# Performance work log

Hardware: AMD Instinct MI355X
Metric: run time of the kernel (lower is better)

## Reference

```python
import jax, jax.numpy as jnp
import numpy as np

# Static dims (match init_kwargs / input_specs)
N, F, C, H, W = 1, 60, 31, 64, 64
DIM = 60          # embed dim == F
WS = 8            # window_size
NH = 6            # num_heads
HD = DIM // NH    # head dim = 10
SHIFT = WS // 2   # shift for odd blocks
NWIN_TOK = WS * WS
MLP_HID = 4 * DIM
EPS = 1e-5


def _rel_pos_index(ws):
    # standard Swin relative position index, computed once in numpy
    coords = np.stack(np.meshgrid(np.arange(ws), np.arange(ws), indexing='ij'))  # (2, ws, ws)
    coords = coords.reshape(2, -1)                                                # (2, ws*ws)
    rel = coords[:, :, None] - coords[:, None, :]                                 # (2, n, n)
    rel = rel.transpose(1, 2, 0)
    rel[..., 0] += ws - 1
    rel[..., 1] += ws - 1
    rel[..., 0] *= 2 * ws - 1
    return rel.sum(-1)                                                            # (n, n)

RPI = jnp.asarray(_rel_pos_index(WS))  # (64, 64) int


def _attn_mask(h, w, ws, shift):
    # mask for shifted-window attention: -100 where tokens come from different regions
    img = np.zeros((h, w))
    cnt = 0
    for hs in (slice(0, -ws), slice(-ws, -shift), slice(-shift, None)):
        for wsl in (slice(0, -ws), slice(-ws, -shift), slice(-shift, None)):
            img[hs, wsl] = cnt
            cnt += 1
    m = img.reshape(h // ws, ws, w // ws, ws).transpose(0, 2, 1, 3).reshape(-1, ws * ws)  # (nW, n)
    diff = m[:, None, :] - m[:, :, None]
    return jnp.asarray(np.where(diff != 0, -100.0, 0.0).astype(np.float32))               # (nW, n, n)

ATTN_MASK = _attn_mask(H, W, WS, SHIFT)


def _ln(x, g, b):
    mu = jnp.mean(x, axis=-1, keepdims=True)
    var = jnp.mean(jnp.square(x - mu), axis=-1, keepdims=True)
    return (x - mu) * jax.lax.rsqrt(var + EPS) * g + b


def _swin_block(x, shift, g1, b1, qkv_w, qkv_b, rpb, proj_w, proj_b,
                g2, b2, fc1_w, fc1_b, fc2_w, fc2_b):
    # x: (B, L=H*W, DIM)
    B = x.shape[0]
    shortcut = x
    h = _ln(x, g1, b1).reshape(B, H, W, DIM)
    if shift > 0:
        h = jnp.roll(h, (-shift, -shift), axis=(1, 2))
    # window partition -> (B*nW, n, DIM)
    win = h.reshape(B, H // WS, WS, W // WS, WS, DIM).transpose(0, 1, 3, 2, 4, 5)
    win = win.reshape(-1, NWIN_TOK, DIM)
    Bw = win.shape[0]
    # qkv projection (torch Linear: y = x @ W.T + b)
    qkv = win @ qkv_w.T + qkv_b                                   # (Bw, n, 3*DIM)
    qkv = qkv.reshape(Bw, NWIN_TOK, 3, NH, HD).transpose(2, 0, 3, 1, 4)
    q, k, v = qkv[0], qkv[1], qkv[2]                              # (Bw, NH, n, HD)
    scale = HD ** -0.5
    attn = jnp.einsum('bhnd,bhmd->bhnm', q * scale, k)            # (Bw, NH, n, n)
    bias = rpb[RPI.reshape(-1)].reshape(NWIN_TOK, NWIN_TOK, NH).transpose(2, 0, 1)
    attn = attn + bias[None]
    if shift > 0:
        nW = ATTN_MASK.shape[0]
        attn = attn.reshape(-1, nW, NH, NWIN_TOK, NWIN_TOK) + ATTN_MASK[None, :, None]
        attn = attn.reshape(-1, NH, NWIN_TOK, NWIN_TOK)
    attn = jax.nn.softmax(attn, axis=-1)
    out = jnp.einsum('bhnm,bhmd->bhnd', attn, v).transpose(0, 2, 1, 3).reshape(Bw, NWIN_TOK, DIM)
    out = out @ proj_w.T + proj_b
    # window reverse -> (B, H, W, DIM)
    out = out.reshape(B, H // WS, W // WS, WS, WS, DIM).transpose(0, 1, 3, 2, 4, 5)
    out = out.reshape(B, H, W, DIM)
    if shift > 0:
        out = jnp.roll(out, (shift, shift), axis=(1, 2))
    x = shortcut + out.reshape(B, H * W, DIM)
    # MLP with exact GELU (torch nn.GELU default)
    h2 = _ln(x, g2, b2)
    h2 = jax.nn.gelu(h2 @ fc1_w.T + fc1_b, approximate=False) @ fc2_w.T + fc2_b
    return x + h2


def setup_inputs() -> dict:
    key = jax.random.key(0)
    ks = jax.random.split(key, 16)
    s = 0.02
    inp = {
        'x': jax.random.normal(ks[0], (N, F, C, H, W), jnp.float32),
        'norm1_g': jnp.ones((2, DIM), jnp.float32),
        'norm1_b': jnp.zeros((2, DIM), jnp.float32),
        'qkv_w': jax.random.normal(ks[1], (2, 3 * DIM, DIM), jnp.float32) * s,
        'qkv_b': jnp.zeros((2, 3 * DIM), jnp.float32),
        'rpb': jax.random.normal(ks[2], (2, (2 * WS - 1) ** 2, NH), jnp.float32) * s,
        'proj_w': jax.random.normal(ks[3], (2, DIM, DIM), jnp.float32) * s,
        'proj_b': jnp.zeros((2, DIM), jnp.float32),
        'norm2_g': jnp.ones((2, DIM), jnp.float32),
        'norm2_b': jnp.zeros((2, DIM), jnp.float32),
        'fc1_w': jax.random.normal(ks[4], (2, MLP_HID, DIM), jnp.float32) * s,
        'fc1_b': jnp.zeros((2, MLP_HID), jnp.float32),
        'fc2_w': jax.random.normal(ks[5], (2, DIM, MLP_HID), jnp.float32) * s,
        'fc2_b': jnp.zeros((2, DIM), jnp.float32),
    }
    return inp


def reference(x, norm1_g, norm1_b, qkv_w, qkv_b, rpb, proj_w, proj_b,
              norm2_g, norm2_b, fc1_w, fc1_b, fc2_w, fc2_b):
    # (N, F, C, H, W) -> (N*C, F, H, W) -> patch embed (flatten) -> (B, L, DIM)
    out = jnp.transpose(x, (0, 2, 1, 3, 4)).reshape(N * C, F, H, W)
    out = out.reshape(N * C, F, H * W).transpose(0, 2, 1)  # (B, L, DIM)
    for i in range(2):
        shift = 0 if i % 2 == 0 else SHIFT
        out = _swin_block(out, shift,
                          norm1_g[i], norm1_b[i], qkv_w[i], qkv_b[i], rpb[i],
                          proj_w[i], proj_b[i], norm2_g[i], norm2_b[i],
                          fc1_w[i], fc1_b[i], fc2_w[i], fc2_b[i])
    # patch unembed -> (B, F, H, W) -> (N, C, F, H, W) -> transpose(1,2)
    out = out.transpose(0, 2, 1).reshape(N * C, F, H, W)
    out = out.reshape(N, C, F, H, W)
    return jnp.transpose(out, (0, 2, 1, 3, 4))
```

## Files before the change

kernel.cpp:

```cpp
#include <hip/hip_runtime.h>
#include <math.h>


#define NB 31
#define NTOK 4096
#define DIM 60
#define NTOT (NB*NTOK)
#define QK_SCALE 0.31622776601683794f

typedef __attribute__((ext_vector_type(8))) short bf16x8;
typedef __attribute__((ext_vector_type(4))) float f32x4;

__device__ __forceinline__ short f2b(float f){
    union{float f;unsigned u;}v; v.f=f;
    unsigned r=(v.u+0x7FFFu+((v.u>>16)&1u))>>16; return (short)r;
}
__device__ __forceinline__ float b2f(unsigned short u){
    union{unsigned u;float f;}v; v.u=((unsigned)u)<<16; return v.f;
}
__device__ __forceinline__ unsigned pk2(float a,float b){
    return (unsigned)(unsigned short)f2b(a) | ((unsigned)(unsigned short)f2b(b)<<16);
}

#define MFMA16(a,b,c) __builtin_amdgcn_mfma_f32_16x16x32_bf16(a,b,c,0,0,0)

#define PK_QKV   0
#define PK_PROJ  13824
#define PK_W1    18432
#define PK_W2    35712
#define PK_BIAS  52608
#define PK_STRIDE 150912

__global__ __launch_bounds__(256) void pack_w(
    const float* __restrict__ qkv_w, const float* __restrict__ proj_w,
    const float* __restrict__ fc1_w, const float* __restrict__ fc2_w,
    const float* __restrict__ rpb, short* __restrict__ pk)
{
    const int L = blockIdx.x;
    short* o = pk + (size_t)L * PK_STRIDE;
    const float* qw = qkv_w + L * 10800;
    const float* pw = proj_w + L * 3600;
    const float* w1 = fc1_w + L * 14400;
    const float* w2 = fc2_w + L * 14400;
    const float* rp = rpb + L * 1350;
    const int t0 = blockIdx.y * 256 + threadIdx.x;
    const int STP = 256 * 8;

    for (int i = t0; i < 192 * 72; i += STP) {
        int row = i / 72, k = i - row * 72;
        int p = row / 96, rg = row - p * 96;
        short v = 0;
        if (rg < 90 && k < 60) {
            int which = rg / 30, idx = rg - which * 30;
            int h = p * 3 + idx / 10, e = idx - (idx / 10) * 10;
            v = f2b(qw[(which * 60 + h * 10 + e) * 60 + k]);
        }
        o[PK_QKV + i] = v;
    }
    for (int i = t0; i < 64 * 72; i += STP) {
        int n = i / 72, k = i - n * 72;
        o[PK_PROJ + i] = (n < 60 && k < 60) ? f2b(pw[n * 60 + k]) : (short)0;
    }
    for (int i = t0; i < 240 * 72; i += STP) {
        int n = i / 72, k = i - n * 72;
        o[PK_W1 + i] = (k < 60) ? f2b(w1[n * 60 + k]) : (short)0;
    }
    for (int i = t0; i < 64 * 264; i += STP) {
        int n = i / 264, k = i - n * 264;
        o[PK_W2 + i] = (n < 60 && k < 240) ? f2b(w2[n * 240 + k]) : (short)0;
    }
    for (int i = t0; i < 4 * 6 * 4096; i += STP) {
        int c = i >> 14, rem = i & 16383;
        int h = rem >> 12; rem &= 4095;
        int j = rem >> 6, ii = rem & 63;
        int iy = ii >> 3, ix = ii & 7, jy = j >> 3, jx = j & 7;
        float v = rp[((iy - jy + 7) * 15 + (ix - jx + 7)) * 6 + h];
        int wyv = (c & 2) ? 7 : 0, wxv = (c & 1) ? 7 : 0;
        int riy = wyv < 7 ? 0 : (iy < 4 ? 1 : 2);
        int rix = wxv < 7 ? 0 : (ix < 4 ? 1 : 2);
        int rjy = wyv < 7 ? 0 : (jy < 4 ? 1 : 2);
        int rjx = wxv < 7 ? 0 : (jx < 4 ? 1 : 2);
        if (riy * 3 + rix != rjy * 3 + rjx) v -= 100.f;
        o[PK_BIAS + i] = f2b(v);
    }
}

template<int L>
__global__ __launch_bounds__(256, 4) void swin_layer(
    const void* __restrict__ xin_v, void* __restrict__ xout_v,
    const float* __restrict__ g1, const float* __restrict__ b1,
    const float* __restrict__ g2, const float* __restrict__ b2,
    const short* __restrict__ pk,
    const float* __restrict__ qkv_b, const float* __restrict__ proj_b,
    const float* __restrict__ fc1_b, const float* __restrict__ fc2_b)
{
    __shared__ __attribute__((aligned(16))) short S[19328];
    short (*xnY)[72]  = (short(*)[72]) S;
    short (*qk2)[104] = (short(*)[104])(S + 4608);
    short (*vTf)[72]  = (short(*)[72]) (S + 11264);
    short (*oac)[72]  = (short(*)[72]) (S + 14720);
    short (*hb)[136]  = (short(*)[136])(S + 4608);
    short (*ln2)[72]  = oac;

    const bf16x8 Z8 = {0,0,0,0,0,0,0,0};
    const f32x4  Z4 = {0.f,0.f,0.f,0.f};

    const int tid = threadIdx.x, blk = blockIdx.x;
    const int b = blk >> 6, w = blk & 63, wy = w >> 3, wx = w & 7;
    const int shift = L ? 4 : 0;
    const int cls = L ? (((wy == 7) ? 2 : 0) + ((wx == 7) ? 1 : 0)) : 0;

    const float* xf = (const float*)xin_v;
    const unsigned short* xb = (const unsigned short*)xin_v;

    for (int i = tid; i < 64 * 36; i += 256) {
        int row = i / 36, z = i - row * 36;
        int bc = z / 6, rem = z - bc * 6;
        qk2[row][bc * 16 + 10 + rem] = 0;
    }
    for (int i = tid; i < 128; i += 256) {
        int row = i >> 1;
        *(int*)&oac[row][60 + ((i & 1) << 1)] = 0;
    }
    {
        const int tk = tid >> 2, l4 = tid & 3;
        const int ty = tk >> 3, tx = tk & 7;
        const int tok = (((wy * 8 + ty + shift) & 63) << 6) + ((wx * 8 + tx + shift) & 63);
        float xr[15]; float s = 0.f, s2 = 0.f;
#pragma unroll
        for (int dd = 0; dd < 15; ++dd) {
            float v;
            if (L == 0) v = xf[(size_t)(dd * 4 + l4) * NTOT + b * NTOK + tok];
            else        v = b2f(xb[((size_t)b * NTOK + tok) * DIM + dd * 4 + l4]);
            xr[dd] = v; s += v; s2 += v * v;
        }
        s  += __shfl_xor(s, 1);  s  += __shfl_xor(s, 2);
        s2 += __shfl_xor(s2, 1); s2 += __shfl_xor(s2, 2);
        const float mu = s * (1.f / 60.f);
        const float rs = rsqrtf(s2 * (1.f / 60.f) - mu * mu + 1e-5f);
#pragma unroll
        for (int dd = 0; dd < 15; ++dd) {
            int d = dd * 4 + l4;
            xnY[tk][d] = f2b((xr[dd] - mu) * rs * g1[d] + b1[d]);
        }
#pragma unroll
        for (int u = 0; u < 3; ++u) xnY[tk][60 + l4 * 3 + u] = 0;
    }

    const int lane = tid & 63;
    const int r16 = lane & 15, g = lane >> 4;
    const int m0 = (tid >> 6) << 4;

    int tok4[4];
#pragma unroll
    for (int r = 0; r < 4; ++r) {
        int row = m0 + g * 4 + r;
        tok4[r] = (((wy * 8 + (row >> 3) + shift) & 63) << 6)
                + ((wx * 8 + (row & 7) + shift) & 63);
    }

    bf16x8 a0 = *(const bf16x8*)&xnY[m0 + r16][g * 8];
    bf16x8 a1 = *(const bf16x8*)&xnY[m0 + r16][32 + g * 8];

    const unsigned short* bbase =
        (const unsigned short*)(pk + PK_BIAS) + cls * 24576 + (m0 + r16) + g * 256;

    for (int p = 0; p < 2; ++p) {
#pragma unroll
        for (int nt = 0; nt < 6; ++nt) {
            const short* wr = pk + PK_QKV + (size_t)(p * 96 + nt * 16 + r16) * 72;
            bf16x8 w0 = *(const bf16x8*)(wr + g * 8);
            bf16x8 w1v = *(const bf16x8*)(wr + 32 + g * 8);
            f32x4 acc = MFMA16(a0, w0, Z4);
            acc = MFMA16(a1, w1v, acc);
            int c = nt * 16 + r16;
            if (c < 90) {
                int which = c / 30, idx = c - which * 30;
                int hl = idx / 10, e = idx - hl * 10;
                float bias = qkv_b[which * 60 + (p * 3 + hl) * 10 + e];
                if (which == 0) {
#pragma unroll
                    for (int r = 0; r < 4; ++r)
                        qk2[m0 + g * 4 + r][hl * 16 + e] = f2b((acc[r] + bias) * QK_SCALE);
                } else if (which == 1) {
#pragma unroll
                    for (int r = 0; r < 4; ++r)
                        qk2[m0 + g * 4 + r][48 + hl * 16 + e] = f2b(acc[r] + bias);
                } else {
#pragma unroll
                    for (int r = 0; r < 2; ++r)
                        *(unsigned*)&vTf[hl * 16 + e][m0 + g * 4 + r * 2] =
                            pk2(acc[r * 2] + bias, acc[r * 2 + 1] + bias);
                }
            }
        }
        __syncthreads();

        for (int hl = 0; hl < 3; ++hl) {
            const int h = p * 3 + hl;
            bf16x8 qa = Z8;
            if (g < 2) qa = *(const bf16x8*)&qk2[m0 + r16][hl * 16 + g * 8];
            f32x4 sv[4];
#pragma unroll
            for (int nt = 0; nt < 4; ++nt) {
                bf16x8 kb = Z8;
                if (g < 2) kb = *(const bf16x8*)&qk2[nt * 16 + r16][48 + hl * 16 + g * 8];
                sv[nt] = MFMA16(kb, qa, Z4);
            }
            const unsigned short* bp = bbase + h * 4096;
#pragma unroll
            for (int nt = 0; nt < 4; ++nt)
#pragma unroll
                for (int r = 0; r < 4; ++r)
                    sv[nt][r] += b2f(bp[nt * 1024 + r * 64]);
            float mx = -1e30f;
#pragma unroll
            for (int nt = 0; nt < 4; ++nt)
#pragma unroll
                for (int r = 0; r < 4; ++r) mx = fmaxf(mx, sv[nt][r]);
            mx = fmaxf(mx, __shfl_xor(mx, 16));
            mx = fmaxf(mx, __shfl_xor(mx, 32));
            float sum = 0.f;
#pragma unroll
            for (int nt = 0; nt < 4; ++nt)
#pragma unroll
                for (int r = 0; r < 4; ++r) {
                    float e = __expf(sv[nt][r] - mx);
                    sv[nt][r] = e; sum += e;
                }
            sum += __shfl_xor(sum, 16);
            sum += __shfl_xor(sum, 32);
            const float inv = 1.f / sum;
            unsigned qd00 = pk2(sv[0][0], sv[0][1]), qd01 = pk2(sv[0][2], sv[0][3]);
            unsigned qd10 = pk2(sv[1][0], sv[1][1]), qd11 = pk2(sv[1][2], sv[1][3]);
            unsigned qd20 = pk2(sv[2][0], sv[2][1]), qd21 = pk2(sv[2][2], sv[2][3]);
            unsigned qd30 = pk2(sv[3][0], sv[3][1]), qd31 = pk2(sv[3][2], sv[3][3]);
            const int sA = (r16 + ((g & 1) << 5)) << 2;
            const int sB = sA + 64;
            const bool hi = (g >> 1) & 1;
            union { unsigned u[4]; bf16x8 v; } pb0, pb1;
            {
                unsigned x0 = __builtin_amdgcn_ds_bpermute(sA, (int)qd00);
                unsigned y0 = __builtin_amdgcn_ds_bpermute(sA, (int)qd10);
                pb0.u[0] = hi ? y0 : x0;
                unsigned x1 = __builtin_amdgcn_ds_bpermute(sA, (int)qd01);
                unsigned y1 = __builtin_amdgcn_ds_bpermute(sA, (int)qd11);
                pb0.u[1] = hi ? y1 : x1;
                unsigned x2 = __builtin_amdgcn_ds_bpermute(sB, (int)qd00);
                unsigned y2 = __builtin_amdgcn_ds_bpermute(sB, (int)qd10);
                pb0.u[2] = hi ? y2 : x2;
                unsigned x3 = __builtin_amdgcn_ds_bpermute(sB, (int)qd01);
                unsigned y3 = __builtin_amdgcn_ds_bpermute(sB, (int)qd11);
                pb0.u[3] = hi ? y3 : x3;
                unsigned u0 = __builtin_amdgcn_ds_bpermute(sA, (int)qd20);
                unsigned v0 = __builtin_amdgcn_ds_bpermute(sA, (int)qd30);
                pb1.u[0] = hi ? v0 : u0;
                unsigned u1 = __builtin_amdgcn_ds_bpermute(sA, (int)qd21);
                unsigned v1 = __builtin_amdgcn_ds_bpermute(sA, (int)qd31);
                pb1.u[1] = hi ? v1 : u1;
                unsigned u2 = __builtin_amdgcn_ds_bpermute(sB, (int)qd20);
                unsigned v2 = __builtin_amdgcn_ds_bpermute(sB, (int)qd30);
                pb1.u[2] = hi ? v2 : u2;
                unsigned u3 = __builtin_amdgcn_ds_bpermute(sB, (int)qd21);
                unsigned v3 = __builtin_amdgcn_ds_bpermute(sB, (int)qd31);
                pb1.u[3] = hi ? v3 : u3;
            }
            bf16x8 va0 = *(const bf16x8*)&vTf[hl * 16 + r16][g * 8];
            bf16x8 va1 = *(const bf16x8*)&vTf[hl * 16 + r16][32 + g * 8];
            f32x4 o = MFMA16(va0, pb0.v, Z4);
            o = MFMA16(va1, pb1.v, o);
            if (g < 2) {
                *(unsigned*)&oac[m0 + r16][h * 10 + g * 4]     = pk2(o[0] * inv, o[1] * inv);
                *(unsigned*)&oac[m0 + r16][h * 10 + g * 4 + 2] = pk2(o[2] * inv, o[3] * inv);
            } else if (g == 2) {
                *(unsigned*)&oac[m0 + r16][h * 10 + 8] = pk2(o[0] * inv, o[1] * inv);
            }
        }
        __syncthreads();
    }

    {
        bf16x8 oa0 = *(const bf16x8*)&oac[m0 + r16][g * 8];
        bf16x8 oa1 = *(const bf16x8*)&oac[m0 + r16][32 + g * 8];
#pragma unroll
        for (int nt = 0; nt < 4; ++nt) {
            const short* wr = pk + PK_PROJ + (size_t)(nt * 16 + r16) * 72;
            bf16x8 w0 = *(const bf16x8*)(wr + g * 8);
            bf16x8 w1v = *(const bf16x8*)(wr + 32 + g * 8);
            f32x4 acc = MFMA16(oa0, w0, Z4);
            acc = MFMA16(oa1, w1v, acc);
            int d = nt * 16 + r16;
            if (d < 60) {
                float bias = proj_b[d];
#pragma unroll
                for (int r = 0; r < 4; ++r) {
                    float res;
                    if (L == 0) res = xf[(size_t)d * NTOT + b * NTOK + tok4[r]];
                    else        res = b2f(xb[((size_t)b * NTOK + tok4[r]) * DIM + d]);
                    xnY[m0 + g * 4 + r][d] = f2b(res + acc[r] + bias);
                }
            }
        }
    }

    {
        const int tk = tid >> 2, l4 = tid & 3;
        float yr[15]; float s = 0.f, s2 = 0.f;
#pragma unroll
        for (int dd = 0; dd < 15; ++dd) {
            float v = b2f((unsigned short)xnY[tk][dd * 4 + l4]);
            yr[dd] = v; s += v; s2 += v * v;
        }
        s  += __shfl_xor(s, 1);  s  += __shfl_xor(s, 2);
        s2 += __shfl_xor(s2, 1); s2 += __shfl_xor(s2, 2);
        const float mu = s * (1.f / 60.f);
        const float rs = rsqrtf(s2 * (1.f / 60.f) - mu * mu + 1e-5f);
#pragma unroll
        for (int dd = 0; dd < 15; ++dd) {
            int d = dd * 4 + l4;
            ln2[tk][d] = f2b((yr[dd] - mu) * rs * g2[d] + b2[d]);
        }
#pragma unroll
        for (int u = 0; u < 3; ++u) ln2[tk][60 + l4 * 3 + u] = 0;
    }
    __syncthreads();

    bf16x8 la0 = *(const bf16x8*)&ln2[m0 + r16][g * 8];
    bf16x8 la1 = *(const bf16x8*)&ln2[m0 + r16][32 + g * 8];
    f32x4 acc2[4];
#pragma unroll
    for (int nt = 0; nt < 4; ++nt) acc2[nt] = Z4;

#pragma unroll
    for (int nt = 0; nt < 8; ++nt) {
        const short* wr = pk + PK_W1 + (size_t)(nt * 16 + r16) * 72;
        bf16x8 w0 = *(const bf16x8*)(wr + g * 8);
        bf16x8 w1v = *(const bf16x8*)(wr + 32 + g * 8);
        f32x4 acc = MFMA16(la0, w0, Z4);
        acc = MFMA16(la1, w1v, acc);
        int c = nt * 16 + r16;
        float bias = fc1_b[c];
#pragma unroll
        for (int r = 0; r < 4; ++r) {
            float u = acc[r] + bias;
            float zz = 1.5957691216057308f * u + 0.07135481178528657f * (u * u * u);
            float ge = u * __builtin_amdgcn_rcpf(1.f + __expf(-zz));
            hb[m0 + g * 4 + r][c] = f2b(ge);
        }
    }
#pragma unroll
    for (int kk = 0; kk < 4; ++kk) {
        bf16x8 ha = *(const bf16x8*)&hb[m0 + r16][kk * 32 + g * 8];
#pragma unroll
        for (int nt = 0; nt < 4; ++nt) {
            const short* wr = pk + PK_W2 + (size_t)(nt * 16 + r16) * 264 + kk * 32 + g * 8;
            acc2[nt] = MFMA16(ha, *(const bf16x8*)wr, acc2[nt]);
        }
    }
    *(int*)&hb[m0 + r16][112 + g * 4]     = 0;
    *(int*)&hb[m0 + r16][112 + g * 4 + 2] = 0;
#pragma unroll
    for (int nt = 0; nt < 7; ++nt) {
        const short* wr = pk + PK_W1 + (size_t)(128 + nt * 16 + r16) * 72;
        bf16x8 w0 = *(const bf16x8*)(wr + g * 8);
        bf16x8 w1v = *(const bf16x8*)(wr + 32 + g * 8);
        f32x4 acc = MFMA16(la0, w0, Z4);
        acc = MFMA16(la1, w1v, acc);
        int c = nt * 16 + r16;
        float bias = fc1_b[128 + c];
#pragma unroll
        for (int r = 0; r < 4; ++r) {
            float u = acc[r] + bias;
            float zz = 1.5957691216057308f * u + 0.07135481178528657f * (u * u * u);
            float ge = u * __builtin_amdgcn_rcpf(1.f + __expf(-zz));
            hb[m0 + g * 4 + r][c] = f2b(ge);
        }
    }
#pragma unroll
    for (int kk = 0; kk < 4; ++kk) {
        bf16x8 ha = *(const bf16x8*)&hb[m0 + r16][kk * 32 + g * 8];
#pragma unroll
        for (int nt = 0; nt < 4; ++nt) {
            const short* wr = pk + PK_W2 + (size_t)(nt * 16 + r16) * 264 + 128 + kk * 32 + g * 8;
            acc2[nt] = MFMA16(ha, *(const bf16x8*)wr, acc2[nt]);
        }
    }
#pragma unroll
    for (int nt = 0; nt < 4; ++nt) {
        int d = nt * 16 + r16;
        if (d < 60) {
            float bias = fc2_b[d];
#pragma unroll
            for (int r = 0; r < 4; ++r) {
                float yv = b2f((unsigned short)xnY[m0 + g * 4 + r][d]);
                float v = yv + acc2[nt][r] + bias;
                if (L == 0)
                    ((unsigned short*)xout_v)[((size_t)b * NTOK + tok4[r]) * DIM + d] =
                        (unsigned short)f2b(v);
                else
                    ((float*)xout_v)[(size_t)d * NTOT + b * NTOK + tok4[r]] = v;
            }
        }
    }
}

extern "C" void kernel_launch(void* const* d_in, const int* in_sizes, int n_in,
                              void* d_out, int out_size, void* d_ws, size_t ws_size,
                              hipStream_t stream)
{
    const float* x       = (const float*)d_in[0];
    const float* norm1_g = (const float*)d_in[1];
    const float* norm1_b = (const float*)d_in[2];
    const float* qkv_w   = (const float*)d_in[3];
    const float* qkv_b   = (const float*)d_in[4];
    const float* rpb     = (const float*)d_in[5];
    const float* proj_w  = (const float*)d_in[6];
    const float* proj_b  = (const float*)d_in[7];
    const float* norm2_g = (const float*)d_in[8];
    const float* norm2_b = (const float*)d_in[9];
    const float* fc1_w   = (const float*)d_in[10];
    const float* fc1_b   = (const float*)d_in[11];
    const float* fc2_w   = (const float*)d_in[12];
    const float* fc2_b   = (const float*)d_in[13];

    unsigned short* bufA = (unsigned short*)d_ws;
    short* pk = (short*)((char*)d_ws + (size_t)NTOT * DIM * 2);

    dim3 block(256);
    pack_w<<<dim3(2, 8), block, 0, stream>>>(qkv_w, proj_w, fc1_w, fc2_w, rpb, pk);

    dim3 grid(NB * 64);
    swin_layer<0><<<grid, block, 0, stream>>>(
        (const void*)x, (void*)bufA,
        norm1_g, norm1_b, norm2_g, norm2_b, pk,
        qkv_b, proj_b, fc1_b, fc2_b);
    swin_layer<1><<<grid, block, 0, stream>>>(
        (const void*)bufA, d_out,
        norm1_g + 60, norm1_b + 60, norm2_g + 60, norm2_b + 60, pk + PK_STRIDE,
        qkv_b + 180, proj_b + 60, fc1_b + 240, fc2_b + 60);

    (void)in_sizes; (void)n_in; (void)out_size; (void)ws_size;
}
```

Before: 201.1 us.

## Stage outputs through LDS for coalesced stores and fold biases into MFMA accumulators

The attention bias plus mask table is now stored as fp32 in a transposed layout, so each lane loads it as a vector and uses it directly as the MFMA accumulator init. The QK scale is folded into the packed Q weights, and the qkv, proj, fc1 and fc2 biases all seed the accumulators instead of being added afterwards. The bf16 input of layer 1 is read with packed 32-bit loads. Final outputs are staged in shared memory and written with coalesced loops instead of scattered per-element stores. Shared memory is split into two smaller regions and occupancy is raised to 5 blocks per CU. The fp32 bias table doubles that buffer's size, and bf16 rounding now uses the library intrinsic.

Result: faster. 178.2 us (-11.4%).

```diff
diff --git a/kernel.cpp b/kernel.cpp
--- a/kernel.cpp
+++ b/kernel.cpp
@@ -1,4 +1,5 @@
 #include <hip/hip_runtime.h>
+#include <hip/hip_bf16.h>
 #include <math.h>
 
 
@@ -12,8 +13,7 @@
 typedef __attribute__((ext_vector_type(4))) float f32x4;
 
 __device__ __forceinline__ short f2b(float f){
-    union{float f;unsigned u;}v; v.f=f;
-    unsigned r=(v.u+0x7FFFu+((v.u>>16)&1u))>>16; return (short)r;
+    return __builtin_bit_cast(short, __float2bfloat16(f));
 }
 __device__ __forceinline__ float b2f(unsigned short u){
     union{unsigned u;float f;}v; v.u=((unsigned)u)<<16; return v.f;
@@ -21,20 +21,18 @@
 __device__ __forceinline__ unsigned pk2(float a,float b){
     return (unsigned)(unsigned short)f2b(a) | ((unsigned)(unsigned short)f2b(b)<<16);
 }
-
 #define MFMA16(a,b,c) __builtin_amdgcn_mfma_f32_16x16x32_bf16(a,b,c,0,0,0)
 
-#define PK_QKV   0
-#define PK_PROJ  13824
-#define PK_W1    18432
-#define PK_W2    35712
-#define PK_BIAS  52608
-#define PK_STRIDE 150912
+#define PK_QKV  0
+#define PK_PROJ 13824
+#define PK_W1   18432
+#define PK_W2   35712
+#define PK_STRIDE 52608
 
 __global__ __launch_bounds__(256) void pack_w(
     const float* __restrict__ qkv_w, const float* __restrict__ proj_w,
     const float* __restrict__ fc1_w, const float* __restrict__ fc2_w,
-    const float* __restrict__ rpb, short* __restrict__ pk)
+    const float* __restrict__ rpb, short* __restrict__ pk, float* __restrict__ btab)
 {
     const int L = blockIdx.x;
     short* o = pk + (size_t)L * PK_STRIDE;
@@ -53,7 +51,9 @@
         if (rg < 90 && k < 60) {
             int which = rg / 30, idx = rg - which * 30;
             int h = p * 3 + idx / 10, e = idx - (idx / 10) * 10;
-            v = f2b(qw[(which * 60 + h * 10 + e) * 60 + k]);
+            float wv = qw[(which * 60 + h * 10 + e) * 60 + k];
+            if (which == 0) wv *= QK_SCALE;
+            v = f2b(wv);
         }
         o[PK_QKV + i] = v;
     }
@@ -69,41 +69,36 @@
         int n = i / 264, k = i - n * 264;
         o[PK_W2 + i] = (n < 60 && k < 240) ? f2b(w2[n * 240 + k]) : (short)0;
     }
-    for (int i = t0; i < 4 * 6 * 4096; i += STP) {
-        int c = i >> 14, rem = i & 16383;
-        int h = rem >> 12; rem &= 4095;
-        int j = rem >> 6, ii = rem & 63;
+    float* bo = btab + (size_t)L * 4 * 24576;
+    for (int i = t0; i < 4 * 24576; i += STP) {
+        int c = i / 24576, rem = i - c * 24576;
+        int h = rem >> 12, rem2 = rem & 4095;
+        int ii = rem2 >> 6, j = rem2 & 63;
         int iy = ii >> 3, ix = ii & 7, jy = j >> 3, jx = j & 7;
         float v = rp[((iy - jy + 7) * 15 + (ix - jx + 7)) * 6 + h];
-        int wyv = (c & 2) ? 7 : 0, wxv = (c & 1) ? 7 : 0;
-        int riy = wyv < 7 ? 0 : (iy < 4 ? 1 : 2);
-        int rix = wxv < 7 ? 0 : (ix < 4 ? 1 : 2);
-        int rjy = wyv < 7 ? 0 : (jy < 4 ? 1 : 2);
-        int rjx = wxv < 7 ? 0 : (jx < 4 ? 1 : 2);
-        if (riy * 3 + rix != rjy * 3 + rjx) v -= 100.f;
-        o[PK_BIAS + i] = f2b(v);
+        int riy = (c & 2) ? (iy < 4 ? 1 : 2) : 0;
+        int rix = (c & 1) ? (ix < 4 ? 1 : 2) : 0;
+        int rjy = (c & 2) ? (jy < 4 ? 1 : 2) : 0;
+        int rjx = (c & 1) ? (jx < 4 ? 1 : 2) : 0;
+        if (riy != rjy || rix != rjx) v -= 100.f;
+        bo[i] = v;
     }
 }
 
 template<int L>
-__global__ __launch_bounds__(256, 4) void swin_layer(
+__global__ __launch_bounds__(256, 5) void swin_layer(
     const void* __restrict__ xin_v, void* __restrict__ xout_v,
     const float* __restrict__ g1, const float* __restrict__ b1,
     const float* __restrict__ g2, const float* __restrict__ b2,
-    const short* __restrict__ pk,
+    const short* __restrict__ pk, const float* __restrict__ btab,
     const float* __restrict__ qkv_b, const float* __restrict__ proj_b,
     const float* __restrict__ fc1_b, const float* __restrict__ fc2_b)
 {
-    __shared__ __attribute__((aligned(16))) short S[19328];
-    short (*xnY)[72]  = (short(*)[72]) S;
-    short (*qk2)[104] = (short(*)[104])(S + 4608);
-    short (*vTf)[72]  = (short(*)[72]) (S + 11264);
-    short (*oac)[72]  = (short(*)[72]) (S + 14720);
-    short (*hb)[136]  = (short(*)[136])(S + 4608);
-    short (*ln2)[72]  = oac;
-
-    const bf16x8 Z8 = {0,0,0,0,0,0,0,0};
-    const f32x4  Z4 = {0.f,0.f,0.f,0.f};
+    __shared__ __attribute__((aligned(16))) short R1[64 * 72];
+    __shared__ __attribute__((aligned(16))) short R2[10112];
+
+    const f32x4 Z4 = {0.f, 0.f, 0.f, 0.f};
+    const bf16x8 Z8 = {0, 0, 0, 0, 0, 0, 0, 0};
 
     const int tid = threadIdx.x, blk = blockIdx.x;
     const int b = blk >> 6, w = blk & 63, wy = w >> 3, wx = w & 7;
@@ -113,25 +108,23 @@
     const float* xf = (const float*)xin_v;
     const unsigned short* xb = (const unsigned short*)xin_v;
 
-    for (int i = tid; i < 64 * 36; i += 256) {
-        int row = i / 36, z = i - row * 36;
-        int bc = z / 6, rem = z - bc * 6;
-        qk2[row][bc * 16 + 10 + rem] = 0;
-    }
-    for (int i = tid; i < 128; i += 256) {
-        int row = i >> 1;
-        *(int*)&oac[row][60 + ((i & 1) << 1)] = 0;
-    }
-    {
-        const int tk = tid >> 2, l4 = tid & 3;
-        const int ty = tk >> 3, tx = tk & 7;
-        const int tok = (((wy * 8 + ty + shift) & 63) << 6) + ((wx * 8 + tx + shift) & 63);
+    for (int i = tid; i < 64 * 18; i += 256) {
+        int row = i / 18, t = i - row * 18, bc = t / 3, k = t - bc * 3;
+        *(int*)&R2[row * 104 + bc * 16 + 10 + 2 * k] = 0;
+    }
+    for (int i = tid; i < 3 * 216; i += 256) {
+        int hl = i / 216, j = i - hl * 216;
+        *(int*)&R2[6656 + (hl * 16 + 10) * 72 + 2 * j] = 0;
+    }
+
+    const int tk = tid >> 2, l4 = tid & 3;
+    const int tok = (((wy * 8 + (tk >> 3) + shift) & 63) << 6)
+                  + ((wx * 8 + (tk & 7) + shift) & 63);
+    if (L == 0) {
         float xr[15]; float s = 0.f, s2 = 0.f;
 #pragma unroll
         for (int dd = 0; dd < 15; ++dd) {
-            float v;
-            if (L == 0) v = xf[(size_t)(dd * 4 + l4) * NTOT + b * NTOK + tok];
-            else        v = b2f(xb[((size_t)b * NTOK + tok) * DIM + dd * 4 + l4]);
+            float v = xf[(size_t)(l4 * 15 + dd) * NTOT + b * NTOK + tok];
             xr[dd] = v; s += v; s2 += v * v;
         }
         s  += __shfl_xor(s, 1);  s  += __shfl_xor(s, 2);
@@ -140,15 +133,45 @@
         const float rs = rsqrtf(s2 * (1.f / 60.f) - mu * mu + 1e-5f);
 #pragma unroll
         for (int dd = 0; dd < 15; ++dd) {
-            int d = dd * 4 + l4;
-            xnY[tk][d] = f2b((xr[dd] - mu) * rs * g1[d] + b1[d]);
-        }
-#pragma unroll
-        for (int u = 0; u < 3; ++u) xnY[tk][60 + l4 * 3 + u] = 0;
-    }
-
-    const int lane = tid & 63;
-    const int r16 = lane & 15, g = lane >> 4;
+            int d = l4 * 15 + dd;
+            R1[tk * 72 + d] = f2b((xr[dd] - mu) * rs * g1[d] + b1[d]);
+        }
+#pragma unroll
+        for (int u = 0; u < 3; ++u) R1[tk * 72 + 60 + l4 * 3 + u] = 0;
+    } else {
+        float xr[16]; float s = 0.f, s2 = 0.f;
+        const int nd = (l4 == 3) ? 6 : 8, c0 = l4 * 16;
+        const unsigned* rp_ = (const unsigned*)(xb + ((size_t)b * NTOK + tok) * DIM) + l4 * 8;
+#pragma unroll
+        for (int j = 0; j < 8; ++j) {
+            if (j < nd) {
+                unsigned u = rp_[j];
+                float v0 = b2f((unsigned short)(u & 0xffff));
+                float v1 = b2f((unsigned short)(u >> 16));
+                xr[2 * j] = v0; xr[2 * j + 1] = v1;
+                s += v0 + v1; s2 += v0 * v0 + v1 * v1;
+            }
+        }
+        s  += __shfl_xor(s, 1);  s  += __shfl_xor(s, 2);
+        s2 += __shfl_xor(s2, 1); s2 += __shfl_xor(s2, 2);
+        const float mu = s * (1.f / 60.f);
+        const float rs = rsqrtf(s2 * (1.f / 60.f) - mu * mu + 1e-5f);
+#pragma unroll
+        for (int j = 0; j < 8; ++j) {
+            if (j < nd) {
+                int d = c0 + 2 * j;
+                float n0 = (xr[2 * j] - mu) * rs * g1[d] + b1[d];
+                float n1 = (xr[2 * j + 1] - mu) * rs * g1[d + 1] + b1[d + 1];
+                *(unsigned*)&R1[tk * 72 + d] = pk2(n0, n1);
+            }
+        }
+        if (l4 == 3) {
+#pragma unroll
+            for (int u = 0; u < 3; ++u) *(unsigned*)&R1[tk * 72 + 60 + 2 * u] = 0;
+        }
+    }
+
+    const int lane = tid & 63, r16 = lane & 15, g = lane >> 4;
     const int m0 = (tid >> 6) << 4;
 
     int tok4[4];
@@ -159,11 +182,9 @@
                 + ((wx * 8 + (row & 7) + shift) & 63);
     }
 
-    bf16x8 a0 = *(const bf16x8*)&xnY[m0 + r16][g * 8];
-    bf16x8 a1 = *(const bf16x8*)&xnY[m0 + r16][32 + g * 8];
-
-    const unsigned short* bbase =
-        (const unsigned short*)(pk + PK_BIAS) + cls * 24576 + (m0 + r16) + g * 256;
+    bf16x8 a0 = *(const bf16x8*)&R1[(m0 + r16) * 72 + g * 8];
+    bf16x8 a1 = *(const bf16x8*)&R1[(m0 + r16) * 72 + 32 + g * 8];
+    const float* btc = btab + (size_t)cls * 24576 + (m0 + r16) * 64;
 
     for (int p = 0; p < 2; ++p) {
 #pragma unroll
@@ -171,26 +192,31 @@
             const short* wr = pk + PK_QKV + (size_t)(p * 96 + nt * 16 + r16) * 72;
             bf16x8 w0 = *(const bf16x8*)(wr + g * 8);
             bf16x8 w1v = *(const bf16x8*)(wr + 32 + g * 8);
-            f32x4 acc = MFMA16(a0, w0, Z4);
+            int c = nt * 16 + r16;
+            int which = 0, hl = 0, e = 0; float bias = 0.f;
+            if (c < 90) {
+                which = c / 30; int idx = c - which * 30;
+                hl = idx / 10; e = idx - hl * 10;
+                bias = qkv_b[which * 60 + (p * 3 + hl) * 10 + e];
+                if (which == 0) bias *= QK_SCALE;
+            }
+            f32x4 acc = {bias, bias, bias, bias};
+            acc = MFMA16(a0, w0, acc);
             acc = MFMA16(a1, w1v, acc);
-            int c = nt * 16 + r16;
             if (c < 90) {
-                int which = c / 30, idx = c - which * 30;
-                int hl = idx / 10, e = idx - hl * 10;
-                float bias = qkv_b[which * 60 + (p * 3 + hl) * 10 + e];
                 if (which == 0) {
 #pragma unroll
                     for (int r = 0; r < 4; ++r)
-                        qk2[m0 + g * 4 + r][hl * 16 + e] = f2b((acc[r] + bias) * QK_SCALE);
+                        R2[(m0 + g * 4 + r) * 104 + hl * 16 + e] = f2b(acc[r]);
                 } else if (which == 1) {
 #pragma unroll
                     for (int r = 0; r < 4; ++r)
-                        qk2[m0 + g * 4 + r][48 + hl * 16 + e] = f2b(acc[r] + bias);
+                        R2[(m0 + g * 4 + r) * 104 + 48 + hl * 16 + e] = f2b(acc[r]);
                 } else {
 #pragma unroll
                     for (int r = 0; r < 2; ++r)
-                        *(unsigned*)&vTf[hl * 16 + e][m0 + g * 4 + r * 2] =
-                            pk2(acc[r * 2] + bias, acc[r * 2 + 1] + bias);
+                        *(unsigned*)&R2[6656 + (hl * 16 + e) * 72 + m0 + g * 4 + 2 * r] =
+                            pk2(acc[2 * r], acc[2 * r + 1]);
                 }
             }
         }
@@ -199,20 +225,15 @@
         for (int hl = 0; hl < 3; ++hl) {
             const int h = p * 3 + hl;
             bf16x8 qa = Z8;
-            if (g < 2) qa = *(const bf16x8*)&qk2[m0 + r16][hl * 16 + g * 8];
+            if (g < 2) qa = *(const bf16x8*)&R2[(m0 + r16) * 104 + hl * 16 + g * 8];
+            const float* bh = btc + h * 4096;
             f32x4 sv[4];
 #pragma unroll
             for (int nt = 0; nt < 4; ++nt) {
                 bf16x8 kb = Z8;
-                if (g < 2) kb = *(const bf16x8*)&qk2[nt * 16 + r16][48 + hl * 16 + g * 8];
-                sv[nt] = MFMA16(kb, qa, Z4);
-            }
-            const unsigned short* bp = bbase + h * 4096;
-#pragma unroll
-            for (int nt = 0; nt < 4; ++nt)
-#pragma unroll
-                for (int r = 0; r < 4; ++r)
-                    sv[nt][r] += b2f(bp[nt * 1024 + r * 64]);
+                if (g < 2) kb = *(const bf16x8*)&R2[(nt * 16 + r16) * 104 + 48 + hl * 16 + g * 8];
+                sv[nt] = MFMA16(kb, qa, *(const f32x4*)&bh[nt * 16 + g * 4]);
+            }
             float mx = -1e30f;
 #pragma unroll
             for (int nt = 0; nt < 4; ++nt)
@@ -231,6 +252,7 @@
             sum += __shfl_xor(sum, 16);
             sum += __shfl_xor(sum, 32);
             const float inv = 1.f / sum;
+
             unsigned qd00 = pk2(sv[0][0], sv[0][1]), qd01 = pk2(sv[0][2], sv[0][3]);
             unsigned qd10 = pk2(sv[1][0], sv[1][1]), qd11 = pk2(sv[1][2], sv[1][3]);
             unsigned qd20 = pk2(sv[2][0], sv[2][1]), qd21 = pk2(sv[2][2], sv[2][3]);
@@ -265,50 +287,50 @@
                 unsigned v3 = __builtin_amdgcn_ds_bpermute(sB, (int)qd31);
                 pb1.u[3] = hi ? v3 : u3;
             }
-            bf16x8 va0 = *(const bf16x8*)&vTf[hl * 16 + r16][g * 8];
-            bf16x8 va1 = *(const bf16x8*)&vTf[hl * 16 + r16][32 + g * 8];
+            bf16x8 va0 = *(const bf16x8*)&R2[6656 + (hl * 16 + r16) * 72 + g * 8];
+            bf16x8 va1 = *(const bf16x8*)&R2[6656 + (hl * 16 + r16) * 72 + 32 + g * 8];
             f32x4 o = MFMA16(va0, pb0.v, Z4);
             o = MFMA16(va1, pb1.v, o);
             if (g < 2) {
-                *(unsigned*)&oac[m0 + r16][h * 10 + g * 4]     = pk2(o[0] * inv, o[1] * inv);
-                *(unsigned*)&oac[m0 + r16][h * 10 + g * 4 + 2] = pk2(o[2] * inv, o[3] * inv);
+                *(unsigned*)&R1[(m0 + r16) * 72 + h * 10 + g * 4]     = pk2(o[0] * inv, o[1] * inv);
+                *(unsigned*)&R1[(m0 + r16) * 72 + h * 10 + g * 4 + 2] = pk2(o[2] * inv, o[3] * inv);
             } else if (g == 2) {
-                *(unsigned*)&oac[m0 + r16][h * 10 + 8] = pk2(o[0] * inv, o[1] * inv);
+                *(unsigned*)&R1[(m0 + r16) * 72 + h * 10 + 8] = pk2(o[0] * inv, o[1] * inv);
             }
         }
         __syncthreads();
     }
 
     {
-        bf16x8 oa0 = *(const bf16x8*)&oac[m0 + r16][g * 8];
-        bf16x8 oa1 = *(const bf16x8*)&oac[m0 + r16][32 + g * 8];
+        bf16x8 oa0 = *(const bf16x8*)&R1[(m0 + r16) * 72 + g * 8];
+        bf16x8 oa1 = *(const bf16x8*)&R1[(m0 + r16) * 72 + 32 + g * 8];
 #pragma unroll
         for (int nt = 0; nt < 4; ++nt) {
             const short* wr = pk + PK_PROJ + (size_t)(nt * 16 + r16) * 72;
             bf16x8 w0 = *(const bf16x8*)(wr + g * 8);
             bf16x8 w1v = *(const bf16x8*)(wr + 32 + g * 8);
-            f32x4 acc = MFMA16(oa0, w0, Z4);
+            int d = nt * 16 + r16;
+            float pb_ = (d < 60) ? proj_b[d] : 0.f;
+            f32x4 acc = {pb_, pb_, pb_, pb_};
+            acc = MFMA16(oa0, w0, acc);
             acc = MFMA16(oa1, w1v, acc);
-            int d = nt * 16 + r16;
             if (d < 60) {
-                float bias = proj_b[d];
 #pragma unroll
                 for (int r = 0; r < 4; ++r) {
                     float res;
                     if (L == 0) res = xf[(size_t)d * NTOT + b * NTOK + tok4[r]];
                     else        res = b2f(xb[((size_t)b * NTOK + tok4[r]) * DIM + d]);
-                    xnY[m0 + g * 4 + r][d] = f2b(res + acc[r] + bias);
+                    R1[(m0 + g * 4 + r) * 72 + d] = f2b(res + acc[r]);
                 }
             }
         }
     }
 
     {
-        const int tk = tid >> 2, l4 = tid & 3;
         float yr[15]; float s = 0.f, s2 = 0.f;
 #pragma unroll
         for (int dd = 0; dd < 15; ++dd) {
-            float v = b2f((unsigned short)xnY[tk][dd * 4 + l4]);
+            float v = b2f((unsigned short)R1[tk * 72 + dd * 4 + l4]);
             yr[dd] = v; s += v; s2 += v * v;
         }
         s  += __shfl_xor(s, 1);  s  += __shfl_xor(s, 2);
@@ -318,88 +340,109 @@
 #pragma unroll
         for (int dd = 0; dd < 15; ++dd) {
             int d = dd * 4 + l4;
-            ln2[tk][d] = f2b((yr[dd] - mu) * rs * g2[d] + b2[d]);
-        }
-#pragma unroll
-        for (int u = 0; u < 3; ++u) ln2[tk][60 + l4 * 3 + u] = 0;
-    }
-    __syncthreads();
-
-    bf16x8 la0 = *(const bf16x8*)&ln2[m0 + r16][g * 8];
-    bf16x8 la1 = *(const bf16x8*)&ln2[m0 + r16][32 + g * 8];
+            R2[tk * 136 + d] = f2b((yr[dd] - mu) * rs * g2[d] + b2[d]);
+        }
+#pragma unroll
+        for (int u = 0; u < 3; ++u) R2[tk * 136 + 60 + l4 * 3 + u] = 0;
+    }
+
+    bf16x8 la0 = *(const bf16x8*)&R2[(m0 + r16) * 136 + g * 8];
+    bf16x8 la1 = *(const bf16x8*)&R2[(m0 + r16) * 136 + 32 + g * 8];
+
     f32x4 acc2[4];
 #pragma unroll
-    for (int nt = 0; nt < 4; ++nt) acc2[nt] = Z4;
+    for (int nt = 0; nt < 4; ++nt) {
+        int d = nt * 16 + r16;
+        float fb = (d < 60) ? fc2_b[d] : 0.f;
+        acc2[nt] = (f32x4){fb, fb, fb, fb};
+    }
 
 #pragma unroll
     for (int nt = 0; nt < 8; ++nt) {
         const short* wr = pk + PK_W1 + (size_t)(nt * 16 + r16) * 72;
         bf16x8 w0 = *(const bf16x8*)(wr + g * 8);
         bf16x8 w1v = *(const bf16x8*)(wr + 32 + g * 8);
-        f32x4 acc = MFMA16(la0, w0, Z4);
+        int c = nt * 16 + r16;
+        float fb = fc1_b[c];
+        f32x4 acc = {fb, fb, fb, fb};
+        acc = MFMA16(la0, w0, acc);
         acc = MFMA16(la1, w1v, acc);
-        int c = nt * 16 + r16;
-        float bias = fc1_b[c];
 #pragma unroll
         for (int r = 0; r < 4; ++r) {
-            float u = acc[r] + bias;
+            float u = acc[r];
             float zz = 1.5957691216057308f * u + 0.07135481178528657f * (u * u * u);
             float ge = u * __builtin_amdgcn_rcpf(1.f + __expf(-zz));
-            hb[m0 + g * 4 + r][c] = f2b(ge);
+            R2[(m0 + g * 4 + r) * 136 + c] = f2b(ge);
         }
     }
 #pragma unroll
     for (int kk = 0; kk < 4; ++kk) {
-        bf16x8 ha = *(const bf16x8*)&hb[m0 + r16][kk * 32 + g * 8];
+        bf16x8 ha = *(const bf16x8*)&R2[(m0 + r16) * 136 + kk * 32 + g * 8];
 #pragma unroll
         for (int nt = 0; nt < 4; ++nt) {
             const short* wr = pk + PK_W2 + (size_t)(nt * 16 + r16) * 264 + kk * 32 + g * 8;
             acc2[nt] = MFMA16(ha, *(const bf16x8*)wr, acc2[nt]);
         }
     }
-    *(int*)&hb[m0 + r16][112 + g * 4]     = 0;
-    *(int*)&hb[m0 + r16][112 + g * 4 + 2] = 0;
+    *(int*)&R2[(m0 + r16) * 136 + 112 + g * 4]     = 0;
+    *(int*)&R2[(m0 + r16) * 136 + 112 + g * 4 + 2] = 0;
 #pragma unroll
     for (int nt = 0; nt < 7; ++nt) {
         const short* wr = pk + PK_W1 + (size_t)(128 + nt * 16 + r16) * 72;
         bf16x8 w0 = *(const bf16x8*)(wr + g * 8);
         bf16x8 w1v = *(const bf16x8*)(wr + 32 + g * 8);
-        f32x4 acc = MFMA16(la0, w0, Z4);
+        int c = nt * 16 + r16;
+        float fb = fc1_b[128 + c];
+        f32x4 acc = {fb, fb, fb, fb};
+        acc = MFMA16(la0, w0, acc);
         acc = MFMA16(la1, w1v, acc);
-        int c = nt * 16 + r16;
-        float bias = fc1_b[128 + c];
 #pragma unroll
         for (int r = 0; r < 4; ++r) {
-            float u = acc[r] + bias;
+            float u = acc[r];
             float zz = 1.5957691216057308f * u + 0.07135481178528657f * (u * u * u);
             float ge = u * __builtin_amdgcn_rcpf(1.f + __expf(-zz));
-            hb[m0 + g * 4 + r][c] = f2b(ge);
+            R2[(m0 + g * 4 + r) * 136 + c] = f2b(ge);
         }
     }
 #pragma unroll
     for (int kk = 0; kk < 4; ++kk) {
-        bf16x8 ha = *(const bf16x8*)&hb[m0 + r16][kk * 32 + g * 8];
+        bf16x8 ha = *(const bf16x8*)&R2[(m0 + r16) * 136 + kk * 32 + g * 8];
 #pragma unroll
         for (int nt = 0; nt < 4; ++nt) {
             const short* wr = pk + PK_W2 + (size_t)(nt * 16 + r16) * 264 + 128 + kk * 32 + g * 8;
             acc2[nt] = MFMA16(ha, *(const bf16x8*)wr, acc2[nt]);
         }
     }
+
 #pragma unroll
     for (int nt = 0; nt < 4; ++nt) {
         int d = nt * 16 + r16;
         if (d < 60) {
-            float bias = fc2_b[d];
 #pragma unroll
             for (int r = 0; r < 4; ++r) {
-                float yv = b2f((unsigned short)xnY[m0 + g * 4 + r][d]);
-                float v = yv + acc2[nt][r] + bias;
-                if (L == 0)
-                    ((unsigned short*)xout_v)[((size_t)b * NTOK + tok4[r]) * DIM + d] =
-                        (unsigned short)f2b(v);
-                else
-                    ((float*)xout_v)[(size_t)d * NTOT + b * NTOK + tok4[r]] = v;
-            }
+                float yv = b2f((unsigned short)R1[(m0 + g * 4 + r) * 72 + d]);
+                float v = yv + acc2[nt][r];
+                if (L == 0) R2[(m0 + g * 4 + r) * 136 + d] = f2b(v);
+                else        ((float*)R2)[(m0 + g * 4 + r) * 68 + d] = v;
+            }
+        }
+    }
+    __syncthreads();
+
+    if (L == 0) {
+        unsigned* ob = (unsigned*)xout_v;
+        const size_t gbase = (size_t)b * NTOK * 30;
+        for (int i = tid; i < 1920; i += 256) {
+            int r = i / 30, c = i - r * 30;
+            int gt = ((wy * 8 + (r >> 3)) << 6) + wx * 8 + (r & 7);
+            ob[gbase + (size_t)gt * 30 + c] = *(unsigned*)&R2[r * 136 + 2 * c];
+        }
+    } else {
+        float* of = (float*)xout_v;
+        for (int i = tid; i < 3840; i += 256) {
+            int d = i >> 6, t = i & 63;
+            int gt = (((wy * 8 + (t >> 3) + 4) & 63) << 6) + ((wx * 8 + (t & 7) + 4) & 63);
+            of[(size_t)d * NTOT + b * NTOK + gt] = ((const float*)R2)[t * 68 + d];
         }
     }
 }
@@ -424,19 +467,21 @@
     const float* fc2_b   = (const float*)d_in[13];
 
     unsigned short* bufA = (unsigned short*)d_ws;
-    short* pk = (short*)((char*)d_ws + (size_t)NTOT * DIM * 2);
+    short* pk  = (short*)((char*)d_ws + (size_t)NTOT * DIM * 2);
+    float* btab = (float*)((char*)pk + 2 * PK_STRIDE * 2);
 
     dim3 block(256);
-    pack_w<<<dim3(2, 8), block, 0, stream>>>(qkv_w, proj_w, fc1_w, fc2_w, rpb, pk);
+    pack_w<<<dim3(2, 8), block, 0, stream>>>(qkv_w, proj_w, fc1_w, fc2_w, rpb, pk, btab);
 
     dim3 grid(NB * 64);
     swin_layer<0><<<grid, block, 0, stream>>>(
         (const void*)x, (void*)bufA,
-        norm1_g, norm1_b, norm2_g, norm2_b, pk,
+        norm1_g, norm1_b, norm2_g, norm2_b, pk, btab,
         qkv_b, proj_b, fc1_b, fc2_b);
     swin_layer<1><<<grid, block, 0, stream>>>(
         (const void*)bufA, d_out,
-        norm1_g + 60, norm1_b + 60, norm2_g + 60, norm2_b + 60, pk + PK_STRIDE,
+        norm1_g + 60, norm1_b + 60, norm2_g + 60, norm2_b + 60,
+        pk + PK_STRIDE, btab + 4 * 24576,
         qkv_b + 180, proj_b + 60, fc1_b + 240, fc2_b + 60);
 
     (void)in_sizes; (void)n_in; (void)out_size; (void)ws_size;
```
